# Kernel tuning notes

Hardware: AMD Instinct MI355X
Metric: run time of the kernel (lower is better)

## Reference

```python
import jax, jax.numpy as jnp
import numpy as np

B, C, L = 4, 64, 4096
RED = 4          # reduction -> q/k channels = C // RED = 16
N_HASHES = 4
HASH_BUCKETS = min(L // 4, 32)  # = 32, matches torch code
EPS = 1e-5


def _conv1x1(x, W, b):
    # x: [B, Cin, L], W: [Cout, Cin], b: [Cout]
    return jnp.einsum('bcl,oc->bol', x, W) + b[None, :, None]


def setup_inputs() -> dict:
    key = jax.random.key(0)
    ks = jax.random.split(key, 12)
    Cq = C // RED
    x = jax.random.normal(ks[0], (B, C, L), dtype=jnp.float32)
    hash_idx = jax.random.randint(ks[1], (B, N_HASHES, L), 0, HASH_BUCKETS, dtype=jnp.int32)
    sC = 1.0 / np.sqrt(C)
    Wq = jax.random.normal(ks[2], (Cq, C), dtype=jnp.float32) * sC
    bq = jax.random.normal(ks[3], (Cq,), dtype=jnp.float32) * 0.01
    Wk = jax.random.normal(ks[4], (Cq, C), dtype=jnp.float32) * sC
    bk = jax.random.normal(ks[5], (Cq,), dtype=jnp.float32) * 0.01
    Wv = jax.random.normal(ks[6], (C, C), dtype=jnp.float32) * sC
    bv = jax.random.normal(ks[7], (C,), dtype=jnp.float32) * 0.01
    Wo = jax.random.normal(ks[8], (C, C), dtype=jnp.float32) * sC
    bo = jax.random.normal(ks[9], (C,), dtype=jnp.float32) * 0.01
    gamma = jax.random.normal(ks[10], (1,), dtype=jnp.float32)  # nonzero so attn path matters
    bn_w = jnp.ones((C,), dtype=jnp.float32)
    bn_b = jnp.zeros((C,), dtype=jnp.float32)
    return dict(x=x, hash_idx=hash_idx, Wq=Wq, bq=bq, Wk=Wk, bk=bk,
                Wv=Wv, bv=bv, Wo=Wo, bo=bo, gamma=gamma, bn_w=bn_w, bn_b=bn_b)


def reference(x, hash_idx, Wq, bq, Wk, bk, Wv, bv, Wo, bo, gamma, bn_w, bn_b):
    # 1x1 conv projections
    q = _conv1x1(x, Wq, bq)   # [B, C/RED, L]
    k = _conv1x1(x, Wk, bk)   # [B, C/RED, L]
    v = _conv1x1(x, Wv, bv)   # [B, C, L]

    qT = q.transpose(0, 2, 1)  # [B, L, Cq]
    kT = k.transpose(0, 2, 1)
    vT = v.transpose(0, 2, 1)  # [B, L, C]

    # raw scores are hash-independent; only the bucket mask changes per hash
    scores = jnp.einsum('bic,bjc->bij', qT, kT)  # [B, L, L], no sqrt(d) scaling (matches torch)

    n_hashes = hash_idx.shape[1]
    acc = jnp.zeros_like(vT)
    for h in range(n_hashes):  # small fixed loop
        idx = hash_idx[:, h, :]                       # [B, L]
        mask = idx[:, :, None] == idx[:, None, :]     # same-bucket mask [B, L, L]
        s = jnp.where(mask, scores, -1e9)
        attn = jax.nn.softmax(s, axis=-1)             # within-bucket softmax (diag always valid)
        acc = acc + jnp.einsum('bij,bjc->bic', attn, vT)
    attn_out = (acc / n_hashes).transpose(0, 2, 1)    # [B, C, L], averaged over hashes

    out = _conv1x1(attn_out, Wo, bo)
    out = gamma * out + x                             # residual with learned scalar

    # BatchNorm1d, training mode: biased batch stats over (B, L) per channel
    mean = out.mean(axis=(0, 2), keepdims=True)
    var = out.var(axis=(0, 2), keepdims=True)
    out = (out - mean) * jax.lax.rsqrt(var + EPS)
    out = out * bn_w[None, :, None] + bn_b[None, :, None]
    return out
```

## Files before the change

### kernel.cpp

```cpp
#include <hip/hip_runtime.h>
#include <math.h>

#define Bn 4
#define Cn 64
#define Ln 4096
#define CQ 16
#define NH 4
#define NB 32
#define EPSV 1e-5f

#define MAXS 384
#define CH2 64
#define KSTR 20
#define VSTR 64

#define QSZ   (Bn*Ln*CQ)
#define VSZ   (Bn*Ln*Cn)
#define ACCSZ (Bn*Ln*Cn)
#define NBH   (Bn*NH)

#define OFF_K   QSZ
#define OFF_V   (2*QSZ)
#define OFF_ACC (2*QSZ + VSZ)

#define LOG2E 1.44269504088896f

__global__ __launch_bounds__(256) void proj_kernel(
        const float* __restrict__ x,
        const float* __restrict__ Wq, const float* __restrict__ bq,
        const float* __restrict__ Wk, const float* __restrict__ bk,
        const float* __restrict__ Wv, const float* __restrict__ bv,
        float* __restrict__ q, float* __restrict__ k, float* __restrict__ v) {
    __shared__ float sWt[Cn*32];
    __shared__ float sb[32];
    int tid = threadIdx.x;
    int third = blockIdx.x % 3;
    int pg    = blockIdx.x / 3;
    int rbase = third * 32;
    for (int idx = tid; idx < Cn*32; idx += 256) {
        int rr = idx & 31, c = idx >> 5;
        int r = rbase + rr;
        float w;
        if (r < 16)      w = Wq[r*Cn + c];
        else if (r < 32) w = Wk[(r-16)*Cn + c];
        else             w = Wv[(r-32)*Cn + c];
        sWt[c*32 + rr] = w;
    }
    if (tid < 32) {
        int r = rbase + tid;
        sb[tid] = (r < 16) ? bq[r] : (r < 32 ? bk[r-16] : bv[r-32]);
    }
    __syncthreads();
    int p = tid & 63, og = tid >> 6;
    int gp = pg * 64 + p;
    int b = gp >> 12, l = gp & (Ln - 1);
    const float* xp = &x[b*Cn*Ln + l];
    int rr0 = og * 8;
    float val[8];
    #pragma unroll
    for (int i = 0; i < 8; i++) val[i] = sb[rr0 + i];
    #pragma unroll
    for (int c0 = 0; c0 < Cn; c0 += 8) {
        float xv[8];
        #pragma unroll
        for (int i = 0; i < 8; i++) xv[i] = xp[(c0 + i)*Ln];
        #pragma unroll
        for (int i = 0; i < 8; i++) {
            const float* wrow = &sWt[(c0 + i)*32 + rr0];
            #pragma unroll
            for (int j = 0; j < 8; j++) val[j] = fmaf(wrow[j], xv[i], val[j]);
        }
    }
    int f = third*8 + og*2;
    float4 t0 = make_float4(val[0], val[1], val[2], val[3]);
    float4 t1 = make_float4(val[4], val[5], val[6], val[7]);
    float4* q4 = (float4*)&q[gp*CQ];
    float4* k4 = (float4*)&k[gp*CQ];
    float4* v4 = (float4*)&v[gp*Cn];
    if (f < 4)      { q4[f]   = t0; q4[f+1] = t1; }
    else if (f < 8) { k4[f-4] = t0; k4[f-3] = t1; }
    else            { v4[f-8] = t0; v4[f-7] = t1; }
}

template<int NS, int MODE>
__device__ __forceinline__ void attn_pass(
        int qbase, int S, int b, int h, int tid, int rem,
        const int* list, float* ks, float* vs,
        const float* __restrict__ q, const float* __restrict__ k,
        const float* __restrict__ v, float* __restrict__ acc) {
    int qd = tid >> 2, c4 = tid & 3;
    float4 qr[NS][4];
    float4 o[NS][4];
    float lsum[NS];
    int qi[NS], iqr[NS];
    #pragma unroll
    for (int s = 0; s < NS; s++) {
        qi[s] = qbase + 64*s + qd;
        iqr[s] = 0;
        lsum[s] = 0.f;
        #pragma unroll
        for (int i = 0; i < 4; i++) o[s][i] = make_float4(0.f,0.f,0.f,0.f);
        if (qi[s] < S) {
            iqr[s] = list[qi[s]];
            const float4* qp = (const float4*)&q[((size_t)b*Ln + iqr[s])*CQ];
            #pragma unroll
            for (int i = 0; i < 4; i++) {
                float4 t = qp[i];
                t.x*=LOG2E; t.y*=LOG2E; t.z*=LOG2E; t.w*=LOG2E;
                qr[s][i] = t;
            }
        } else {
            #pragma unroll
            for (int i = 0; i < 4; i++) qr[s][i] = make_float4(0.f,0.f,0.f,0.f);
        }
    }
    for (int cc = 0; cc < S; cc += CH2) {
        int nk = min(CH2, S - cc);
        __syncthreads();
        {
            int jj = tid >> 2, cf = tid & 3;
            if (jj < nk) {
                const float4* kp = (const float4*)&k[((size_t)b*Ln + list[cc+jj])*CQ];
                *(float4*)&ks[jj*KSTR + cf*4] = kp[cf];
            }
        }
        #pragma unroll
        for (int uu = 0; uu < 4; uu++) {
            int idx = uu*256 + tid;
            int jj = idx >> 4, cf = idx & 15;
            if (jj < nk) {
                const float4* vp = (const float4*)&v[((size_t)b*Ln + list[cc+jj])*Cn];
                *(float4*)&vs[jj*VSTR + cf*4] = vp[cf];
            }
        }
        __syncthreads();
        if (rem > 0) {
            for (int j = 0; j < nk; j++) {
                const float4* kr = (const float4*)&ks[j*KSTR];
                float4 k0 = kr[0], k1 = kr[1], k2 = kr[2], k3 = kr[3];
                const float4* vp4 = (const float4*)&vs[j*VSTR + c4*16];
                float4 v0 = vp4[0], v1 = vp4[1], v2 = vp4[2], v3 = vp4[3];
                #pragma unroll
                for (int s = 0; s < NS; s++) {
                    float s0 = qr[s][0].x*k0.x + qr[s][0].y*k0.y + qr[s][0].z*k0.z + qr[s][0].w*k0.w;
                    float s1 = qr[s][1].x*k1.x + qr[s][1].y*k1.y + qr[s][1].z*k1.z + qr[s][1].w*k1.w;
                    float s2 = qr[s][2].x*k2.x + qr[s][2].y*k2.y + qr[s][2].z*k2.z + qr[s][2].w*k2.w;
                    float s3 = qr[s][3].x*k3.x + qr[s][3].y*k3.y + qr[s][3].z*k3.z + qr[s][3].w*k3.w;
                    float pw = __builtin_amdgcn_exp2f((s0 + s1) + (s2 + s3));
                    lsum[s] += pw;
                    o[s][0].x = fmaf(pw, v0.x, o[s][0].x); o[s][0].y = fmaf(pw, v0.y, o[s][0].y);
                    o[s][0].z = fmaf(pw, v0.z, o[s][0].z); o[s][0].w = fmaf(pw, v0.w, o[s][0].w);
                    o[s][1].x = fmaf(pw, v1.x, o[s][1].x); o[s][1].y = fmaf(pw, v1.y, o[s][1].y);
                    o[s][1].z = fmaf(pw, v1.z, o[s][1].z); o[s][1].w = fmaf(pw, v1.w, o[s][1].w);
                    o[s][2].x = fmaf(pw, v2.x, o[s][2].x); o[s][2].y = fmaf(pw, v2.y, o[s][2].y);
                    o[s][2].z = fmaf(pw, v2.z, o[s][2].z); o[s][2].w = fmaf(pw, v2.w, o[s][2].w);
                    o[s][3].x = fmaf(pw, v3.x, o[s][3].x); o[s][3].y = fmaf(pw, v3.y, o[s][3].y);
                    o[s][3].z = fmaf(pw, v3.z, o[s][3].z); o[s][3].w = fmaf(pw, v3.w, o[s][3].w);
                }
            }
        }
    }
    #pragma unroll
    for (int s = 0; s < NS; s++) {
        if (qi[s] < S) {
            float inv = 1.f / lsum[s];
            #pragma unroll
            for (int i = 0; i < 4; i++) {
                o[s][i].x*=inv; o[s][i].y*=inv; o[s][i].z*=inv; o[s][i].w*=inv;
            }
            if (MODE == 1) {
                float4* ap = (float4*)&acc[((size_t)h*Bn*Ln + b*Ln + iqr[s])*Cn + c4*16];
                ap[0]=o[s][0]; ap[1]=o[s][1]; ap[2]=o[s][2]; ap[3]=o[s][3];
            } else {
                float* ap = &acc[((size_t)b*Ln + iqr[s])*Cn + c4*16];
                #pragma unroll
                for (int i = 0; i < 4; i++) {
                    atomicAdd(&ap[4*i+0], (&o[s][i].x)[0]);
                    atomicAdd(&ap[4*i+1], (&o[s][i].x)[1]);
                    atomicAdd(&ap[4*i+2], (&o[s][i].x)[2]);
                    atomicAdd(&ap[4*i+3], (&o[s][i].x)[3]);
                }
            }
        }
    }
}

template<int MODE>
__global__ __launch_bounds__(256, 2) void attn_kernel(
        const float* __restrict__ q, const float* __restrict__ k,
        const float* __restrict__ v, const int* __restrict__ hidx,
        float* __restrict__ acc) {
    __shared__ int list[MAXS];
    __shared__ float ks[CH2*KSTR];
    __shared__ float vs[CH2*VSTR];
    __shared__ int wtot[4];
    int blk = blockIdx.x;
    int u  = blk & (NB-1);
    int bh = blk >> 5;
    int b  = bh >> 2;
    int h  = bh & 3;
    int tid = threadIdx.x;

    const int4* hp4 = (const int4*)(&hidx[bh*Ln] + tid*16);
    int hv[16];
    #pragma unroll
    for (int t = 0; t < 4; t++) {
        int4 tmp = hp4[t];
        hv[t*4+0]=tmp.x; hv[t*4+1]=tmp.y; hv[t*4+2]=tmp.z; hv[t*4+3]=tmp.w;
    }
    int myCnt = 0;
    #pragma unroll
    for (int t = 0; t < 16; t++) myCnt += (hv[t] == u);
    int lane = tid & 63, wv = tid >> 6;
    int pre = myCnt;
    #pragma unroll
    for (int d = 1; d < 64; d <<= 1) {
        int t = __shfl_up(pre, d, 64);
        if (lane >= d) pre += t;
    }
    if (lane == 63) wtot[wv] = pre;
    __syncthreads();
    int base = 0;
    #pragma unroll
    for (int w = 0; w < 4; w++) base += (w < wv) ? wtot[w] : 0;
    int Sall = wtot[0] + wtot[1] + wtot[2] + wtot[3];
    int S = min(Sall, MAXS);
    int excl = base + pre - myCnt;
    #pragma unroll
    for (int t = 0; t < 16; t++) {
        if (hv[t] == u) {
            if (excl < MAXS) list[excl] = tid*16 + t;
            excl++;
        }
    }
    __syncthreads();

    int wq0 = (tid >> 6) << 4;
    for (int qbase = 0; qbase < S; qbase += 192) {
        int rem = S - qbase - wq0;
        if (rem > 128)     attn_pass<3,MODE>(qbase,S,b,h,tid,rem,list,ks,vs,q,k,v,acc);
        else if (rem > 64) attn_pass<2,MODE>(qbase,S,b,h,tid,rem,list,ks,vs,q,k,v,acc);
        else               attn_pass<1,MODE>(qbase,S,b,h,tid,rem,list,ks,vs,q,k,v,acc);
    }
}

template<int MODE>
__global__ __launch_bounds__(256) void outconv_kernel(
        const float* __restrict__ acc, const float* __restrict__ Wo,
        const float* __restrict__ bo, const float* __restrict__ gamma,
        const float* __restrict__ x, float* __restrict__ y) {
    __shared__ float sWt[Cn*Cn];
    __shared__ float sA[Cn*33];
    __shared__ float sb[Cn];
    int tid = threadIdx.x;
    int pg = blockIdx.x;
    for (int idx = tid; idx < Cn*Cn; idx += 256) {
        int o = idx & 63, c = idx >> 6;
        sWt[c*Cn + o] = Wo[o*Cn + c];
    }
    if (tid < Cn) sb[tid] = bo[tid];
    const float4* a4 = (const float4*)&acc[(size_t)pg*32*Cn];
    #pragma unroll
    for (int r = 0; r < 2; r++) {
        int idx = r*256 + tid;
        int p = idx >> 4, c0 = (idx & 15) * 4;
        float4 t = a4[idx];
        if (MODE == 1) {
            float4 t1 = a4[(size_t)ACCSZ/4   + idx];
            float4 t2 = a4[(size_t)ACCSZ/4*2 + idx];
            float4 t3 = a4[(size_t)ACCSZ/4*3 + idx];
            t.x += t1.x + t2.x + t3.x; t.y += t1.y + t2.y + t3.y;
            t.z += t1.z + t2.z + t3.z; t.w += t1.w + t2.w + t3.w;
        }
        sA[(c0+0)*33 + p] = t.x*0.25f;
        sA[(c0+1)*33 + p] = t.y*0.25f;
        sA[(c0+2)*33 + p] = t.z*0.25f;
        sA[(c0+3)*33 + p] = t.w*0.25f;
    }
    __syncthreads();
    float g = gamma[0];
    int p = tid & 31, og = tid >> 5;
    int gp = pg * 32 + p;
    int b = gp >> 12, l = gp & (Ln - 1);
    int o0 = og * 8;
    float val[8];
    #pragma unroll
    for (int i = 0; i < 8; i++) val[i] = sb[o0 + i];
    #pragma unroll
    for (int c = 0; c < Cn; c++) {
        float av = sA[c*33 + p];
        const float* wrow = &sWt[c*Cn + o0];
        #pragma unroll
        for (int i = 0; i < 8; i++) val[i] = fmaf(wrow[i], av, val[i]);
    }
    #pragma unroll
    for (int i = 0; i < 8; i++) {
        int o = o0 + i;
        float yv = fmaf(g, val[i], x[(b*Cn + o)*Ln + l]);
        y[(b*Cn + o)*Ln + l] = yv;
    }
}

__global__ __launch_bounds__(256) void stats_kernel(
        const float* __restrict__ y, float* __restrict__ ssumP, float* __restrict__ ssqP) {
    int c = blockIdx.x >> 2;
    int part = blockIdx.x & 3;
    int tid = threadIdx.x;
    const float4* yp = (const float4*)&y[(part*Cn + c)*Ln];
    float s = 0.f, s2 = 0.f;
    #pragma unroll
    for (int i = 0; i < 4; i++) {
        float4 t = yp[i*256 + tid];
        s  += t.x + t.y + t.z + t.w;
        s2 += t.x*t.x + t.y*t.y + t.z*t.z + t.w*t.w;
    }
    #pragma unroll
    for (int w = 1; w < 64; w <<= 1) {
        s  += __shfl_xor(s,  w, 64);
        s2 += __shfl_xor(s2, w, 64);
    }
    __shared__ float rs[4], rs2[4];
    int wv = tid >> 6;
    if ((tid & 63) == 0) { rs[wv] = s; rs2[wv] = s2; }
    __syncthreads();
    if (tid == 0) {
        ssumP[blockIdx.x] = rs[0]+rs[1]+rs[2]+rs[3];
        ssqP[blockIdx.x]  = rs2[0]+rs2[1]+rs2[2]+rs2[3];
    }
}

__global__ __launch_bounds__(256) void norm_kernel(
        const float* __restrict__ y,
        const float* __restrict__ ssumP, const float* __restrict__ ssqP,
        const float* __restrict__ bnw, const float* __restrict__ bnb,
        float* __restrict__ out) {
    int idx = blockIdx.x * 256 + threadIdx.x;
    int flat = idx * 4;
    int c = (flat / Ln) & 63;
    float s = 0.f, s2 = 0.f;
    #pragma unroll
    for (int hh = 0; hh < 4; hh++) { s += ssumP[c*4+hh]; s2 += ssqP[c*4+hh]; }
    const float n = (float)(Bn*Ln);
    float mu = s / n;
    float var = s2 / n - mu*mu;
    float is = rsqrtf(var + EPSV);
    float w = is * bnw[c];
    float bb = bnb[c] - mu * w;
    float4 t = ((const float4*)y)[idx];
    float4 r;
    r.x = t.x*w + bb; r.y = t.y*w + bb; r.z = t.z*w + bb; r.w = t.w*w + bb;
    ((float4*)out)[idx] = r;
}

extern "C" void kernel_launch(void* const* d_in, const int* in_sizes, int n_in,
                              void* d_out, int out_size, void* d_ws, size_t ws_size,
                              hipStream_t stream) {
    const float* x    = (const float*)d_in[0];
    const int*   hidx = (const int*)  d_in[1];
    const float* Wq   = (const float*)d_in[2];
    const float* bq   = (const float*)d_in[3];
    const float* Wk   = (const float*)d_in[4];
    const float* bk   = (const float*)d_in[5];
    const float* Wv   = (const float*)d_in[6];
    const float* bv   = (const float*)d_in[7];
    const float* Wo   = (const float*)d_in[8];
    const float* bo   = (const float*)d_in[9];
    const float* gam  = (const float*)d_in[10];
    const float* bnw  = (const float*)d_in[11];
    const float* bnb  = (const float*)d_in[12];
    float* out = (float*)d_out;

    float* ws  = (float*)d_ws;
    float* q   = ws;
    float* k   = ws + OFF_K;
    float* v   = ws + OFF_V;
    float* acc = ws + OFF_ACC;
    float* y   = ws;

    const size_t bigNeed = ((size_t)OFF_ACC + 4*(size_t)ACCSZ + 512) * sizeof(float);
    bool big = ws_size >= bigNeed;
    float* ssumP = acc + (big ? 4*(size_t)ACCSZ : (size_t)ACCSZ);
    float* ssqP  = ssumP + 256;

    proj_kernel<<<Bn*Ln/64*3, 256, 0, stream>>>(x, Wq, bq, Wk, bk, Wv, bv, q, k, v);
    if (big) {
        attn_kernel<1><<<NBH*NB, 256, 0, stream>>>(q, k, v, hidx, acc);
        outconv_kernel<1><<<Bn*Ln/32, 256, 0, stream>>>(acc, Wo, bo, gam, x, y);
    } else {
        hipMemsetAsync(acc, 0, (size_t)ACCSZ*sizeof(float), stream);
        attn_kernel<0><<<NBH*NB, 256, 0, stream>>>(q, k, v, hidx, acc);
        outconv_kernel<0><<<Bn*Ln/32, 256, 0, stream>>>(acc, Wo, bo, gam, x, y);
    }
    stats_kernel<<<Cn*4, 256, 0, stream>>>(y, ssumP, ssqP);
    norm_kernel<<<Bn*Cn*Ln/4/256, 256, 0, stream>>>(y, ssumP, ssqP, bnw, bnb, out);
}
```

Measured before the change: 169.3 us.

## Double-buffer K/V shared-memory tiles with register prefetch in attention kernel

```diff
diff --git a/kernel.cpp b/kernel.cpp
--- a/kernel.cpp
+++ b/kernel.cpp
@@ -35,7 +35,6 @@
     __shared__ float sb[32];
     int tid = threadIdx.x;
     int third = blockIdx.x % 3;
-    int pg    = blockIdx.x / 3;
     int rbase = third * 32;
     for (int idx = tid; idx < Cn*32; idx += 256) {
         int rr = idx & 31, c = idx >> 5;
@@ -52,7 +51,7 @@
     }
     __syncthreads();
     int p = tid & 63, og = tid >> 6;
-    int gp = pg * 64 + p;
+    int gp = blockIdx.x / 3 * 64 + p;
     int b = gp >> 12, l = gp & (Ln - 1);
     const float* xp = &x[b*Cn*Ln + l];
     int rr0 = og * 8;
@@ -114,31 +113,57 @@
             for (int i = 0; i < 4; i++) qr[s][i] = make_float4(0.f,0.f,0.f,0.f);
         }
     }
+    int kjj = tid >> 2, kcf = tid & 3;
+    __syncthreads();
+    {
+        int nk = min(CH2, S);
+        if (kjj < nk) {
+            const float4* kp = (const float4*)&k[((size_t)b*Ln + list[kjj])*CQ];
+            *(float4*)&ks[kjj*KSTR + kcf*4] = kp[kcf];
+        }
+        #pragma unroll
+        for (int uu = 0; uu < 4; uu++) {
+            int idx = uu*256 + tid;
+            int jv = idx >> 4, cv = idx & 15;
+            if (jv < nk) {
+                const float4* vp = (const float4*)&v[((size_t)b*Ln + list[jv])*Cn];
+                *(float4*)&vs[jv*VSTR + cv*4] = vp[cv];
+            }
+        }
+    }
+    int cur = 0;
     for (int cc = 0; cc < S; cc += CH2) {
         int nk = min(CH2, S - cc);
         __syncthreads();
-        {
-            int jj = tid >> 2, cf = tid & 3;
-            if (jj < nk) {
-                const float4* kp = (const float4*)&k[((size_t)b*Ln + list[cc+jj])*CQ];
-                *(float4*)&ks[jj*KSTR + cf*4] = kp[cf];
-            }
-        }
-        #pragma unroll
-        for (int uu = 0; uu < 4; uu++) {
-            int idx = uu*256 + tid;
-            int jj = idx >> 4, cf = idx & 15;
-            if (jj < nk) {
-                const float4* vp = (const float4*)&v[((size_t)b*Ln + list[cc+jj])*Cn];
-                *(float4*)&vs[jj*VSTR + cf*4] = vp[cf];
-            }
-        }
-        __syncthreads();
+        int cc2 = cc + CH2;
+        bool hasNext = cc2 < S;
+        int nk2 = S - cc2; if (nk2 > CH2) nk2 = CH2;
+        float4 kreg = make_float4(0.f,0.f,0.f,0.f);
+        float4 vreg[4];
+        #pragma unroll
+        for (int uu = 0; uu < 4; uu++) vreg[uu] = make_float4(0.f,0.f,0.f,0.f);
+        if (hasNext) {
+            if (kjj < nk2) {
+                const float4* kp = (const float4*)&k[((size_t)b*Ln + list[cc2 + kjj])*CQ];
+                kreg = kp[kcf];
+            }
+            #pragma unroll
+            for (int uu = 0; uu < 4; uu++) {
+                int idx = uu*256 + tid;
+                int jv = idx >> 4, cv = idx & 15;
+                if (jv < nk2) {
+                    const float4* vp = (const float4*)&v[((size_t)b*Ln + list[cc2 + jv])*Cn];
+                    vreg[uu] = vp[cv];
+                }
+            }
+        }
+        const float* ksc = ks + cur*(CH2*KSTR);
+        const float* vsc = vs + cur*(CH2*VSTR);
         if (rem > 0) {
             for (int j = 0; j < nk; j++) {
-                const float4* kr = (const float4*)&ks[j*KSTR];
+                const float4* kr = (const float4*)&ksc[j*KSTR];
                 float4 k0 = kr[0], k1 = kr[1], k2 = kr[2], k3 = kr[3];
-                const float4* vp4 = (const float4*)&vs[j*VSTR + c4*16];
+                const float4* vp4 = (const float4*)&vsc[j*VSTR + c4*16];
                 float4 v0 = vp4[0], v1 = vp4[1], v2 = vp4[2], v3 = vp4[3];
                 #pragma unroll
                 for (int s = 0; s < NS; s++) {
@@ -159,6 +184,18 @@
                 }
             }
         }
+        if (hasNext) {
+            float* ksn = ks + (cur^1)*(CH2*KSTR);
+            float* vsn = vs + (cur^1)*(CH2*VSTR);
+            if (kjj < nk2) *(float4*)&ksn[kjj*KSTR + kcf*4] = kreg;
+            #pragma unroll
+            for (int uu = 0; uu < 4; uu++) {
+                int idx = uu*256 + tid;
+                int jv = idx >> 4, cv = idx & 15;
+                if (jv < nk2) *(float4*)&vsn[jv*VSTR + cv*4] = vreg[uu];
+            }
+        }
+        cur ^= 1;
     }
     #pragma unroll
     for (int s = 0; s < NS; s++) {
@@ -191,8 +228,8 @@
         const float* __restrict__ v, const int* __restrict__ hidx,
         float* __restrict__ acc) {
     __shared__ int list[MAXS];
-    __shared__ float ks[CH2*KSTR];
-    __shared__ float vs[CH2*VSTR];
+    __shared__ float ks[2*CH2*KSTR];
+    __shared__ float vs[2*CH2*VSTR];
     __shared__ int wtot[4];
     int blk = blockIdx.x;
     int u  = blk & (NB-1);
```

New measurement: 169.5 us. About the same (+0.1%).
